# Kernel optimization log

Measured on AMD Instinct MI355X. Metric: run time of the kernel, lower is better.

## Reference

```python
import jax, jax.numpy as jnp
import numpy as np

DIM = 128
HEADS = 8
WS = 4  # window_size = size/11 = 44/11
HID = DIM * 4  # ffn_expansion_factor=4


def layernorm_cl(x, w, b):
    # WithBias LayerNorm over channel dim; x: (b,c,h,w)
    x3 = x.transpose(0, 2, 3, 1)  # b,h,w,c
    mu = x3.mean(-1, keepdims=True)
    var = ((x3 - mu) ** 2).mean(-1, keepdims=True)
    y = (x3 - mu) / jnp.sqrt(var + 1e-5) * w + b
    return y.transpose(0, 3, 1, 2)


def win_part(t, ws):
    # (b,c,h,w) -> (b*nh*nw, ws*ws, c), matching torch view/permute/contiguous
    b, c, h, w = t.shape
    t = t.reshape(b, c, h // ws, ws, w // ws, ws)
    t = t.transpose(0, 2, 4, 3, 5, 1)
    return t.reshape(b * (h // ws) * (w // ws), ws * ws, c)


def conv1x1(x, w):
    # w: (Cout, Cin, 1, 1)
    return jnp.einsum('bchw,oc->bohw', x, w[:, :, 0, 0])


def dwconv3(x, w):
    # depthwise 3x3, padding 1; w: (C,1,3,3)
    return jax.lax.conv_general_dilated(
        x, w, window_strides=(1, 1), padding=[(1, 1), (1, 1)],
        dimension_numbers=('NCHW', 'OIHW', 'NCHW'),
        feature_group_count=x.shape[1])


def setup_inputs() -> dict:
    key = jax.random.key(0)
    ks = jax.random.split(key, 10)
    b, c, h, w = 4, DIM, 176, 176
    inp = {
        'x': jax.random.normal(ks[0], (b, c, h, w), jnp.float32),
        'mask': jax.random.uniform(ks[1], (b, 1, 44, 44), jnp.float32),
        'edge': jax.random.normal(ks[2], (b, c, 44, 44), jnp.float32),
        'ln1_w': jnp.ones((c,), jnp.float32),
        'ln1_b': jnp.zeros((c,), jnp.float32),
        'Wq': jax.random.normal(ks[3], (c, c), jnp.float32) * 0.02,
        'Wk': jax.random.normal(ks[4], (c, c), jnp.float32) * 0.02,
        'Wv': jax.random.normal(ks[5], (c, c), jnp.float32) * 0.02,
        'ln2_w': jnp.ones((c,), jnp.float32),
        'ln2_b': jnp.zeros((c,), jnp.float32),
        'w_in': jax.random.normal(ks[6], (2 * HID, c, 1, 1), jnp.float32) * 0.02,
        'w_dw': jax.random.normal(ks[7], (2 * HID, 1, 3, 3), jnp.float32) * 0.1,
        'w_out': jax.random.normal(ks[8], (c, HID, 1, 1), jnp.float32) * 0.02,
    }
    return inp


def _forward(x, mask, edge, ln1_w, ln1_b, Wq, Wk, Wv, ln2_w, ln2_b, w_in, w_dw, w_out):
    b, c, h, w = x.shape
    d = c // HEADS
    scale = d ** (-0.5)

    # --- attention branch ---
    xn = layernorm_cl(x, ln1_w, ln1_b)
    x0 = xn

    edge_r = jax.image.resize(edge, (b, c, h, w), method='bilinear')
    mask_r = jax.image.resize(mask, (b, mask.shape[1], h, w), method='bilinear')

    q = win_part(edge_r, WS) @ Wq.T                 # (Bw, N, c)
    x0w = win_part(x0 * mask_r, WS)
    k = x0w @ Wk.T
    v = x0w @ Wv.T

    Bw, N = q.shape[0], q.shape[1]
    q = q.reshape(Bw, N, HEADS, d)
    k = k.reshape(Bw, N, HEADS, d)
    v = v.reshape(Bw, N, HEADS, d)

    # NB: faithful to original einsum -- contracts over heads axis, giving
    # per-token d x d channel attention.
    dots = jnp.einsum('bnij,bnik->bnjk', q, k) * scale  # (Bw, N, d, d)
    attn = jax.nn.softmax(dots, axis=-1)
    out = jnp.einsum('bnjk,bnik->bnij', attn, v)        # (Bw, N, HEADS, d)
    out = out.reshape(Bw, N, c)

    # faithful (non-inverse) window merge: view -> permute -> view
    out = out.reshape(b, h // WS, w // WS, WS * WS * c)
    out = out.transpose(0, 3, 1, 2).reshape(b, c, h, w)

    x = x + out

    # --- GDFN feedforward ---
    y = layernorm_cl(x, ln2_w, ln2_b)
    y = conv1x1(y, w_in)
    y = dwconv3(y, w_dw)
    y1, y2 = jnp.split(y, 2, axis=1)
    y = jax.nn.gelu(y1, approximate=False) * y2
    y = conv1x1(y, w_out)
    return x + y


def reference(x, mask, edge, ln1_w, ln1_b, Wq, Wk, Wv, ln2_w, ln2_b, w_in, w_dw, w_out):
    return _forward(x, mask, edge, ln1_w, ln1_b, Wq, Wk, Wv, ln2_w, ln2_b, w_in, w_dw, w_out)
```

## Files before the change

kernel.cpp:

```cpp
#include <hip/hip_runtime.h>
#include <hip/hip_bf16.h>
#include <math.h>

typedef __hip_bfloat16 bf16;
typedef short bf16x8 __attribute__((ext_vector_type(8)));
typedef short bf16x4 __attribute__((ext_vector_type(4)));
typedef float floatx4 __attribute__((ext_vector_type(4)));

#define YX 30976
#define NPOS (4*YX)

__device__ __forceinline__ float ldin(const void* p, size_t i, int bf) {
  return bf ? __bfloat162float(((const bf16*)p)[i]) : ((const float*)p)[i];
}

__device__ __forceinline__ void unpack8(bf16x8 v, float* f) {
  const unsigned* u = (const unsigned*)&v;
#pragma unroll
  for (int i = 0; i < 4; ++i) {
    f[2 * i]     = __uint_as_float(u[i] << 16);
    f[2 * i + 1] = __uint_as_float(u[i] & 0xffff0000u);
  }
}

__device__ __forceinline__ void glds16(const void* g, void* l) {
  __builtin_amdgcn_global_load_lds(
      (const __attribute__((address_space(1))) unsigned int*)g,
      (__attribute__((address_space(3))) unsigned int*)l, 16, 0, 0);
}

__device__ __forceinline__ void tap44(int o, int& i0, int& i1, float& f) {
  int t = o >> 2, r = o & 3;
  int base = (r < 2) ? (t - 1) : t;
  f = (r == 0) ? 0.625f : (r == 1) ? 0.875f : (r == 2) ? 0.125f : 0.375f;
  i0 = base < 0 ? 0 : base;
  i1 = (base + 1 > 43) ? 43 : base + 1;
}

__global__ void k_sniff(const unsigned* __restrict__ ln1w, int* __restrict__ flag) {
  if (threadIdx.x == 0 && blockIdx.x == 0)
    *flag = (*ln1w == 0x3F800000u) ? 0 : 1;
}

__global__ void __launch_bounds__(256) k_castw(
    const void* __restrict__ src, bf16* __restrict__ dst, int n,
    const int* __restrict__ flag) {
  int i = blockIdx.x * 256 + threadIdx.x;
  if (i >= n) return;
  int bf = *flag;
  dst[i] = bf ? ((const bf16*)src)[i]
              : __float2bfloat16(((const float*)src)[i]);
}

__global__ void __launch_bounds__(256) k_castdw(
    const void* __restrict__ src, bf16* __restrict__ dst,
    const int* __restrict__ flag) {
  int i = blockIdx.x * 256 + threadIdx.x;
  if (i >= 9216) return;
  int bf = *flag;
  int ch = i & 511, tap = (i >> 9) % 9, g = i / (512 * 9);
  float v = ldin(src, (size_t)(g * 512 + ch) * 9 + tap, bf);
  dst[(g * 9 + tap) * 512 + ch] = __float2bfloat16(v);
}

__global__ void __launch_bounds__(256) k_prep(
    const void* __restrict__ xin, const void* __restrict__ mask,
    const void* __restrict__ edge, const void* __restrict__ ln1w,
    const void* __restrict__ ln1b, const int* __restrict__ flag,
    bf16* __restrict__ e_buf, bf16* __restrict__ xm_buf,
    bf16* __restrict__ x_pm) {
  __shared__ float sP[4][64], ssP[4][64];
  __shared__ float smu[64], srstd[64], smv[64];
  __shared__ float slw[128], slb[128];
  __shared__ __align__(16) bf16 tileE[128 * 68];
  int bf = *flag;
  int tid = threadIdx.x;
  int p0 = blockIdx.x * 64;
  int b = p0 / YX, yx0 = p0 % YX;
  if (tid < 128) { slw[tid] = ldin(ln1w, tid, bf); slb[tid] = ldin(ln1b, tid, bf); }
  int pp = tid & 63, cq = tid >> 6;

  float vals[32], s = 0.f, ss = 0.f;
  {
    size_t base = ((size_t)(b * 128 + cq * 32)) * YX + yx0 + pp;
#pragma unroll
    for (int j = 0; j < 32; ++j) {
      float v = ldin(xin, base + (size_t)j * YX, bf);
      vals[j] = v; s += v; ss += v * v;
    }
  }
  sP[cq][pp] = s; ssP[cq][pp] = ss;
  __syncthreads();

  if (tid < 64) {
    float st  = sP[0][tid] + sP[1][tid] + sP[2][tid] + sP[3][tid];
    float sst = ssP[0][tid] + ssP[1][tid] + ssP[2][tid] + ssP[3][tid];
    float mu = st * (1.f / 128.f);
    float var = sst * (1.f / 128.f) - mu * mu;
    smu[tid] = mu;
    srstd[tid] = rsqrtf(fmaxf(var, 0.f) + 1e-5f);
    int gyx = yx0 + tid, y = gyx / 176, x = gyx % 176;
    int y0, y1, x0, x1; float fy, fx;
    tap44(y, y0, y1, fy); tap44(x, x0, x1, fx);
    size_t mb = (size_t)b * 1936;
    float m00 = ldin(mask, mb + y0 * 44 + x0, bf);
    float m01 = ldin(mask, mb + y0 * 44 + x1, bf);
    float m10 = ldin(mask, mb + y1 * 44 + x0, bf);
    float m11 = ldin(mask, mb + y1 * 44 + x1, bf);
    smv[tid] = (m00 * (1.f - fx) + m01 * fx) * (1.f - fy) +
               (m10 * (1.f - fx) + m11 * fx) * fy;
  }
  __syncthreads();

  {
    float mu = smu[pp], rstd = srstd[pp], mv = smv[pp];
    size_t ob = (size_t)(p0 + pp) * 128 + cq * 32;
#pragma unroll
    for (int j8 = 0; j8 < 4; ++j8) {
      bf16x8 xr, xmr;
#pragma unroll
      for (int i = 0; i < 8; ++i) {
        int j = j8 * 8 + i;
        float v = vals[j];
        int c = cq * 32 + j;
        ((bf16*)&xr)[i]  = __float2bfloat16(v);
        ((bf16*)&xmr)[i] = __float2bfloat16(((v - mu) * rstd * slw[c] + slb[c]) * mv);
      }
      *(bf16x8*)(x_pm + ob + j8 * 8)   = xr;
      *(bf16x8*)(xm_buf + ob + j8 * 8) = xmr;
    }
  }

  {
    int c = tid & 127, half = tid >> 7;
    size_t ebase = (size_t)(b * 128 + c) * 1936;
    int px = half * 32, pxend = px + 32;
    while (px < pxend) {
      int gyx = yx0 + px;
      int y = gyx / 176, x = gyx % 176;
      int seg = pxend - px;
      int rem = 176 - x;
      if (rem < seg) seg = rem;
      int y0, y1; float fy; tap44(y, y0, y1, fy);
      float fy0 = 1.f - fy;
      size_t r0 = ebase + (size_t)y0 * 44, r1 = ebase + (size_t)y1 * 44;
      int t = x >> 2;
      int tm = (t - 1 < 0) ? 0 : t - 1;
      int tp = (t + 1 > 43) ? 43 : t + 1;
      float Rm = fy0 * ldin(edge, r0 + tm, bf) + fy * ldin(edge, r1 + tm, bf);
      float R0 = fy0 * ldin(edge, r0 + t,  bf) + fy * ldin(edge, r1 + t,  bf);
      float Rp = fy0 * ldin(edge, r0 + tp, bf) + fy * ldin(edge, r1 + tp, bf);
      for (int g = 0; g < seg; g += 4) {
        bf16x4 pk;
        ((bf16*)&pk)[0] = __float2bfloat16(0.375f * Rm + 0.625f * R0);
        ((bf16*)&pk)[1] = __float2bfloat16(0.125f * Rm + 0.875f * R0);
        ((bf16*)&pk)[2] = __float2bfloat16(0.875f * R0 + 0.125f * Rp);
        ((bf16*)&pk)[3] = __float2bfloat16(0.625f * R0 + 0.375f * Rp);
        *(bf16x4*)&tileE[c * 68 + px + g] = pk;
        ++t;
        Rm = R0; R0 = Rp;
        int tn = (t + 1 > 43) ? 43 : t + 1;
        Rp = fy0 * ldin(edge, r0 + tn, bf) + fy * ldin(edge, r1 + tn, bf);
      }
      px += seg;
    }
  }
  __syncthreads();

  {
    size_t ob = (size_t)(p0 + pp) * 128 + cq * 32;
#pragma unroll
    for (int j8 = 0; j8 < 4; ++j8) {
      bf16x8 ev;
#pragma unroll
      for (int i = 0; i < 8; ++i)
        ((bf16*)&ev)[i] = tileE[(cq * 32 + j8 * 8 + i) * 68 + pp];
      *(bf16x8*)(e_buf + ob + j8 * 8) = ev;
    }
  }
}

__global__ void __launch_bounds__(384, 3) k_qkvattn(
    const bf16* __restrict__ E, const bf16* __restrict__ XM,
    const bf16* __restrict__ Wq, const bf16* __restrict__ Wk,
    const bf16* __restrict__ Wv, bf16* __restrict__ O) {
  __shared__ __align__(16) bf16 smem[32768];
  int tid = threadIdx.x;
  int wave = tid / 64, lane = tid & 63;
  int mat = wave >> 1, h = wave & 1;
  int l15 = lane & 15, quad = lane >> 4;
  int m0b = blockIdx.x * 64;

  const bf16* gA = (mat == 0) ? E : XM;
  const bf16* gW = (mat == 0) ? Wq : (mat == 1) ? Wk : Wv;

  floatx4 acc[4][4] = {};

#define STAGE(bb, kt)                                                          \
  {                                                                            \
    _Pragma("unroll")                                                          \
    for (int c = 0; c < 4; ++c)                                                \
      glds16(gW + (size_t)(h * 64 + c * 16 + l15) * 128 + (kt) + quad * 8,     \
             smem + (bb) + 4096 + mat * 4096 + (h * 4 + c) * 512);             \
    if (mat == 0) {                                                            \
      _Pragma("unroll")                                                        \
      for (int g = 0; g < 2; ++g) {                                            \
        int mm = h * 2 + g;                                                    \
        glds16(gA + (size_t)(m0b + mm * 16 + l15) * 128 + (kt) + quad * 8,     \
               smem + (bb) + mm * 512);                                        \
      }                                                                        \
    } else {                                                                   \
      int mm = wave - 2;                                                       \
      glds16(gA + (size_t)(m0b + mm * 16 + l15) * 128 + (kt) + quad * 8,       \
             smem + (bb) + 2048 + mm * 512);                                   \
    }                                                                          \
  }

  STAGE(0, 0);
  __syncthreads();

  int cur = 0;
  for (int t = 0; t < 4; ++t) {
    int nb = cur ^ 16384;
    if (t < 3) STAGE(nb, (t + 1) * 32);
    const bf16* sA = smem + cur + (mat ? 2048 : 0);
    const bf16* sW = smem + cur + 4096 + mat * 4096;
    bf16x8 af[4], bfr[4];
#pragma unroll
    for (int m = 0; m < 4; ++m)
      af[m] = *(const bf16x8*)(sA + m * 512 + lane * 8);
#pragma unroll
    for (int n = 0; n < 4; ++n)
      bfr[n] = *(const bf16x8*)(sW + (h * 4 + n) * 512 + lane * 8);
#pragma unroll
    for (int m = 0; m < 4; ++m)
#pragma unroll
      for (int n = 0; n < 4; ++n)
        acc[m][n] = __builtin_amdgcn_mfma_f32_16x16x32_bf16(bfr[n], af[m], acc[m][n], 0, 0, 0);
    __syncthreads();
    cur = nb;
  }
#undef STAGE

  if (mat < 2) {
    bf16* sT = smem + mat * 8192;
    int key = l15 & 7;
#pragma unroll
    for (int m = 0; m < 4; ++m) {
      int tokl = m * 16 + l15;
#pragma unroll
      for (int r = 0; r < 4; ++r) {
        int cidx = quad * 4 + r;
        bf16x4 o;
#pragma unroll
        for (int n = 0; n < 4; ++n) ((bf16*)&o)[n] = __float2bfloat16(acc[m][n][r]);
        *(bf16x4*)(sT + tokl * 128 + ((cidx ^ key) * 8) + h * 4) = o;
      }
    }
  } else {
    float* sVf = (float*)(smem + 16384);
    int key = l15 & 7;
#pragma unroll
    for (int m = 0; m < 4; ++m) {
      int tokl = m * 16 + l15;
#pragma unroll
      for (int n = 0; n < 4; ++n) {
        int ch4 = h * 16 + n * 4 + quad;
        floatx4 o;
#pragma unroll
        for (int r = 0; r < 4; ++r) o[r] = acc[m][n][r];
        *(floatx4*)(sVf + tokl * 128 + ((ch4 ^ key) << 2)) = o;
      }
    }
  }
  __syncthreads();

  const bf16* sQt = smem;
  const bf16* sKt = smem + 8192;
  const float* sVf = (const float*)(smem + 16384);
  for (int round = 0; round < 3; ++round) {
    int item = round * 384 + tid;
    if (item < 1024) {
      int tt = item >> 4, j = item & 15;
      int key = tt & 7;
      float qv[8];
      {
        bf16x8 q8 = *(const bf16x8*)(sQt + tt * 128 + ((j ^ key) * 8));
        unpack8(q8, qv);
      }
      float s[16], mx = -1e30f;
#pragma unroll
      for (int kk = 0; kk < 16; ++kk) {
        bf16x8 k8 = *(const bf16x8*)(sKt + tt * 128 + ((kk ^ key) * 8));
        float kv[8]; unpack8(k8, kv);
        float a = 0.f;
#pragma unroll
        for (int i = 0; i < 8; ++i) a += qv[i] * kv[i];
        a *= 0.25f;
        s[kk] = a; mx = fmaxf(mx, a);
      }
      float sum = 0.f;
#pragma unroll
      for (int kk = 0; kk < 16; ++kk) { s[kk] = __expf(s[kk] - mx); sum += s[kk]; }
      float inv = 1.f / sum;
      bf16x8 ov;
#pragma unroll
      for (int i = 0; i < 8; ++i) {
        float o = 0.f;
#pragma unroll
        for (int c4 = 0; c4 < 4; ++c4) {
          int ch4 = i * 4 + c4;
          floatx4 v4 = *(const floatx4*)(sVf + tt * 128 + ((ch4 ^ key) << 2));
#pragma unroll
          for (int r = 0; r < 4; ++r) o += s[c4 * 4 + r] * v4[r];
        }
        ((bf16*)&ov)[i] = __float2bfloat16(o * inv);
      }
      *(bf16x8*)(O + (size_t)(m0b + tt) * 128 + j * 8) = ov;
    }
  }
}

__global__ void __launch_bounds__(256) k_gemm2(
    const bf16* __restrict__ A, const bf16* __restrict__ W1,
    const bf16* __restrict__ W2, bf16* __restrict__ C1,
    bf16* __restrict__ C2) {
  __shared__ __align__(16) bf16 smem[20480];
  int tid = threadIdx.x;
  int wave = tid >> 6, lane = tid & 63;
  int row = lane & 15, kq8 = (lane >> 4) * 8;
  int m0b = blockIdx.x * 64;

  int srow = lane >> 2, scol = (lane & 3) * 8;
  const bf16* gA = A + (size_t)(m0b + wave * 16 + srow) * 128 + scol;
  const bf16* Wsrc = (wave < 2) ? W1 : W2;
  const bf16* gB = Wsrc + (size_t)((wave & 1) * 64 + srow) * 128 + scol;
  bf16* lA = smem + wave * 512;
  bf16* lB = smem + 2048 + wave * 2048;

  floatx4 acc[4][4] = {};
  glds16(gA, lA);
#pragma unroll
  for (int c = 0; c < 4; ++c) glds16(gB + c * 16 * 128, lB + c * 512);
  __syncthreads();

  int cur = 0;
  for (int t = 0; t < 4; ++t) {
    int nxt = cur ^ 1;
    if (t < 3) {
      const bf16* ga = gA + (t + 1) * 32;
      const bf16* gb = gB + (t + 1) * 32;
      glds16(ga, lA + nxt * 10240);
#pragma unroll
      for (int c = 0; c < 4; ++c)
        glds16(gb + c * 16 * 128, lB + nxt * 10240 + c * 512);
    }
    const bf16* sA = smem + cur * 10240;
    const bf16* sB = sA + 2048;
    bf16x8 af[4], bfr[4];
#pragma unroll
    for (int m = 0; m < 4; ++m)
      af[m] = *(const bf16x8*)(sA + (m * 16 + row) * 32 + kq8);
#pragma unroll
    for (int n = 0; n < 4; ++n)
      bfr[n] = *(const bf16x8*)(sB + (wave * 64 + n * 16 + row) * 32 + kq8);
#pragma unroll
    for (int m = 0; m < 4; ++m)
#pragma unroll
      for (int n = 0; n < 4; ++n)
        acc[m][n] = __builtin_amdgcn_mfma_f32_16x16x32_bf16(bfr[n], af[m], acc[m][n], 0, 0, 0);
    __syncthreads();
    cur = nxt;
  }

  bf16* dst = (wave < 2) ? C1 : C2;
  int j = lane & 15, quad = lane >> 4;
#pragma unroll
  for (int m = 0; m < 4; ++m) {
    size_t pb = (size_t)(m0b + m * 16 + j) * 128 + (wave & 1) * 64 + quad * 4;
#pragma unroll
    for (int n = 0; n < 4; ++n) {
      bf16x4 o;
#pragma unroll
      for (int r = 0; r < 4; ++r) ((bf16*)&o)[r] = __float2bfloat16(acc[m][n][r]);
      *(bf16x4*)(dst + pb + n * 16) = o;
    }
  }
}

__global__ void __launch_bounds__(256) k_merge(
    const bf16* __restrict__ AO2, const bf16* __restrict__ x_pm,
    const void* __restrict__ ln2w, const void* __restrict__ ln2b,
    const int* __restrict__ flag, bf16* __restrict__ resid,
    bf16* __restrict__ yln) {
  __shared__ __align__(16) bf16 stile[64 * 128];
  __shared__ float sP[4][64], ssP[4][64];
  __shared__ float smu[64], srstd[64];
  __shared__ float slw[128], slb[128];
  int bf = *flag;
  int tid = threadIdx.x;
  int bi = blockIdx.x;
  int iw0 = bi % 11, ih = (bi / 11) % 44, b = bi / 484;
  if (tid < 128) { slw[tid] = ldin(ln2w, tid, bf); slb[tid] = ldin(ln2b, tid, bf); }

#pragma unroll
  for (int q = 0; q < 4; ++q) {
    int idx = q * 256 + tid;
    int m = idx & 15, sp = idx >> 4;
    int dy = sp >> 4, wj = (sp >> 2) & 3, dx = sp & 3;
    int ys = ih * 4 + dy, xs = iw0 * 16 + wj * 4 + dx;
    bf16x8 v = *(const bf16x8*)(AO2 + (size_t)((b * 176 + ys) * 176 + xs) * 128 + m * 8);
    int opx = m * 4 + wj, n = dy * 4 + dx;
    *(bf16x8*)&stile[opx * 128 + (n ^ (opx & 15)) * 8] = v;
  }
  __syncthreads();

  int opx = tid & 63, cq = tid >> 6;
  int t = opx >> 2, wj = opx & 3;
  size_t p = (size_t)b * YX + t * 1936 + ih * 44 + iw0 * 4 + wj;
  float vals[32], s = 0.f, ss = 0.f;
#pragma unroll
  for (int j = 0; j < 4; ++j) {
    int nchunk = cq * 4 + j;
    bf16x8 av = *(const bf16x8*)&stile[opx * 128 + (nchunk ^ (opx & 15)) * 8];
    bf16x8 xv = *(const bf16x8*)(x_pm + p * 128 + cq * 32 + j * 8);
    float af[8], xf[8];
    unpack8(av, af); unpack8(xv, xf);
#pragma unroll
    for (int i = 0; i < 8; ++i) {
      float v = af[i] + xf[i];
      vals[j * 8 + i] = v; s += v; ss += v * v;
    }
  }
  sP[cq][opx] = s; ssP[cq][opx] = ss;
  __syncthreads();
  if (tid < 64) {
    float st  = sP[0][tid] + sP[1][tid] + sP[2][tid] + sP[3][tid];
    float sst = ssP[0][tid] + ssP[1][tid] + ssP[2][tid] + ssP[3][tid];
    float mu = st * (1.f / 128.f);
    float var = sst * (1.f / 128.f) - mu * mu;
    smu[tid] = mu;
    srstd[tid] = rsqrtf(fmaxf(var, 0.f) + 1e-5f);
  }
  __syncthreads();

  {
    float mu = smu[opx], rstd = srstd[opx];
    size_t ob = p * 128 + cq * 32;
#pragma unroll
    for (int j8 = 0; j8 < 4; ++j8) {
      bf16x8 rv, yv;
#pragma unroll
      for (int i = 0; i < 8; ++i) {
        int j = j8 * 8 + i;
        float v = vals[j];
        int c = cq * 32 + j;
        ((bf16*)&rv)[i] = __float2bfloat16(v);
        ((bf16*)&yv)[i] = __float2bfloat16((v - mu) * rstd * slw[c] + slb[c]);
      }
      *(bf16x8*)(resid + ob + j8 * 8) = rv;
      *(bf16x8*)(yln + ob + j8 * 8)   = yv;
    }
  }
}

__global__ void __launch_bounds__(256) k_dwgelu(
    const bf16* __restrict__ H1, const bf16* __restrict__ H2,
    const bf16* __restrict__ Wt, int j0, bf16* __restrict__ G) {
  int tid = blockIdx.x * 256 + threadIdx.x;
  int pos = tid >> 4, c8 = (tid & 15) * 8;
  int b = pos / YX, yx = pos % YX, y = yx / 176, x = yx % 176;
  float d1[8] = {}, d2[8] = {};
#pragma unroll
  for (int dy = 0; dy < 3; ++dy) {
    int ny = y + dy - 1;
    if (ny < 0 || ny > 175) continue;
#pragma unroll
    for (int dx = 0; dx < 3; ++dx) {
      int nx = x + dx - 1;
      if (nx < 0 || nx > 175) continue;
      int tap = dy * 3 + dx;
      size_t off = (size_t)(b * YX + ny * 176 + nx) * 128 + c8;
      float h1[8], h2[8], w1[8], w2[8];
      unpack8(*(const bf16x8*)(H1 + off), h1);
      unpack8(*(const bf16x8*)(H2 + off), h2);
      unpack8(*(const bf16x8*)(Wt + tap * 512 + j0 + c8), w1);
      unpack8(*(const bf16x8*)(Wt + (9 + tap) * 512 + j0 + c8), w2);
#pragma unroll
      for (int i = 0; i < 8; ++i) {
        d1[i] += w1[i] * h1[i];
        d2[i] += w2[i] * h2[i];
      }
    }
  }
  bf16x8 outv;
#pragma unroll
  for (int i = 0; i < 8; ++i) {
    float gl = 0.5f * d1[i] * (1.f + erff(d1[i] * 0.70710678118f));
    ((bf16*)&outv)[i] = __float2bfloat16(gl * d2[i]);
  }
  *(bf16x8*)(G + (size_t)pos * 512 + j0 + c8) = outv;
}

__global__ void __launch_bounds__(256) k_gemm_final(
    const bf16* __restrict__ G, const bf16* __restrict__ W,
    const bf16* __restrict__ resid, void* __restrict__ out,
    const int* __restrict__ flag) {
  __shared__ __align__(16) bf16 smem[16384];
  int tid = threadIdx.x;
  int wave = tid >> 6, lane = tid & 63;
  int row = lane & 15, kq8 = (lane >> 4) * 8;
  int wr = wave >> 1, wc = wave & 1;
  int m0b = blockIdx.x * 128;

  int srow = lane >> 2, scol = (lane & 3) * 8;
  const bf16* gA = G + (size_t)(m0b + wave * 32 + srow) * 512 + scol;
  const bf16* gB = W + (size_t)(wave * 32 + srow) * 512 + scol;
  bf16* lA = smem + wave * 1024;
  bf16* lB = smem + 4096 + wave * 1024;

  floatx4 acc[4][4] = {};
  glds16(gA, lA);            glds16(gA + 16 * 512, lA + 512);
  glds16(gB, lB);            glds16(gB + 16 * 512, lB + 512);
  __syncthreads();

  int cur = 0;
  for (int t = 0; t < 16; ++t) {
    int nxt = cur ^ 1;
    if (t < 15) {
      const bf16* ga = gA + (t + 1) * 32;
      const bf16* gb = gB + (t + 1) * 32;
      glds16(ga, lA + nxt * 8192);            glds16(ga + 16 * 512, lA + nxt * 8192 + 512);
      glds16(gb, lB + nxt * 8192);            glds16(gb + 16 * 512, lB + nxt * 8192 + 512);
    }
    const bf16* sA = smem + cur * 8192;
    const bf16* sB = sA + 4096;
    bf16x8 af[4], bfr[4];
#pragma unroll
    for (int m = 0; m < 4; ++m)
      af[m] = *(const bf16x8*)(sA + (wr * 64 + m * 16 + row) * 32 + kq8);
#pragma unroll
    for (int n = 0; n < 4; ++n)
      bfr[n] = *(const bf16x8*)(sB + (wc * 64 + n * 16 + row) * 32 + kq8);
#pragma unroll
    for (int m = 0; m < 4; ++m)
#pragma unroll
      for (int n = 0; n < 4; ++n)
        acc[m][n] = __builtin_amdgcn_mfma_f32_16x16x32_bf16(af[m], bfr[n], acc[m][n], 0, 0, 0);
    __syncthreads();
    cur = nxt;
  }

  {
    const bf16* gR = resid + (size_t)(m0b + wave * 32 + (lane >> 4)) * 128 + (lane & 15) * 8;
    bf16* lR = smem + wave * 32 * 128;
#pragma unroll
    for (int c = 0; c < 8; ++c)
      glds16(gR + (size_t)c * 4 * 128, lR + c * 4 * 128);
  }
  __syncthreads();

  int bfo = *flag;
  int b = m0b / YX, yx0 = m0b % YX;
  int j = lane & 15, quad = lane >> 4;
#pragma unroll
  for (int n = 0; n < 4; ++n) {
    int ch = wc * 64 + n * 16 + j;
    const bf16* rsl = smem + ch;
    size_t cb = (size_t)(b * 128 + ch) * YX + yx0;
#pragma unroll
    for (int m = 0; m < 4; ++m) {
      int pos = wr * 64 + m * 16 + quad * 4;
      float v[4];
#pragma unroll
      for (int r = 0; r < 4; ++r)
        v[r] = acc[m][n][r] + __bfloat162float(rsl[(pos + r) * 128]);
      if (bfo) {
        bf16x4 o;
#pragma unroll
        for (int r = 0; r < 4; ++r) ((bf16*)&o)[r] = __float2bfloat16(v[r]);
        *(bf16x4*)((bf16*)out + cb + pos) = o;
      } else {
        floatx4 o;
#pragma unroll
        for (int r = 0; r < 4; ++r) o[r] = v[r];
        *(floatx4*)((float*)out + cb + pos) = o;
      }
    }
  }
}

extern "C" void kernel_launch(void* const* d_in, const int* in_sizes, int n_in,
                              void* d_out, int out_size, void* d_ws, size_t ws_size,
                              hipStream_t stream) {
  const void* x    = d_in[0];
  const void* mask = d_in[1];
  const void* edge = d_in[2];
  const void* ln1w = d_in[3];
  const void* ln1b = d_in[4];
  const void* Wq   = d_in[5];
  const void* Wk   = d_in[6];
  const void* Wv   = d_in[7];
  const void* ln2w = d_in[8];
  const void* ln2b = d_in[9];
  const void* w_in = d_in[10];
  const void* w_dw = d_in[11];
  const void* w_out= d_in[12];

  char* ws = (char*)d_ws;
  const size_t SEG  = 31719424;
  const size_t GSZ  = 126877696;
  bf16* G     = (bf16*)(ws);
  bf16* B0    = (bf16*)(ws);
  bf16* B1    = (bf16*)(ws + GSZ);
  bf16* H1    = (bf16*)(ws + GSZ + SEG);
  bf16* H2    = (bf16*)(ws + GSZ + 2 * SEG);
  bf16* resid = (bf16*)(ws + GSZ + 3 * SEG);
  char* wsw   = ws + GSZ + 4 * SEG;
  bf16* wq_b   = (bf16*)(wsw);
  bf16* wk_b   = (bf16*)(wsw + 32768);
  bf16* wv_b   = (bf16*)(wsw + 65536);
  bf16* win_b  = (bf16*)(wsw + 98304);
  bf16* wout_b = (bf16*)(wsw + 98304 + 262144);
  bf16* wdwt_b = (bf16*)(wsw + 98304 + 262144 + 131072);
  int* flag    = (int*)(wsw + 98304 + 262144 + 131072 + 32768);

  k_sniff<<<1, 64, 0, stream>>>((const unsigned*)ln1w, flag);
  k_castw<<<64, 256, 0, stream>>>(Wq, wq_b, 16384, flag);
  k_castw<<<64, 256, 0, stream>>>(Wk, wk_b, 16384, flag);
  k_castw<<<64, 256, 0, stream>>>(Wv, wv_b, 16384, flag);
  k_castw<<<512, 256, 0, stream>>>(w_in, win_b, 131072, flag);
  k_castw<<<256, 256, 0, stream>>>(w_out, wout_b, 65536, flag);
  k_castdw<<<36, 256, 0, stream>>>(w_dw, wdwt_b, flag);

  k_prep<<<NPOS / 64, 256, 0, stream>>>(x, mask, edge, ln1w, ln1b, flag,
                                        B0, B1, H1 );
  k_qkvattn<<<NPOS / 64, 384, 0, stream>>>(B0, B1, wq_b, wk_b, wv_b, B0);
  k_merge<<<4 * 44 * 11, 256, 0, stream>>>(B0, H1 , ln2w, ln2b, flag,
                                           resid, B1);
  for (int j0 = 0; j0 < 512; j0 += 128) {
    k_gemm2<<<NPOS / 64, 256, 0, stream>>>(B1, win_b + (size_t)j0 * 128,
                                           win_b + (size_t)(512 + j0) * 128, H1, H2);
    k_dwgelu<<<NPOS * 16 / 256, 256, 0, stream>>>(H1, H2, wdwt_b, j0, G);
  }
  k_gemm_final<<<NPOS / 128, 256, 0, stream>>>(G, wout_b, resid, d_out, flag);
}
```

Measured before the change: 668.8 us.

## Split prep into separate edge-upsample and LayerNorm kernels with wider loads

The fused prep kernel is split into two kernels. k_edge handles one output row per block: it stages the two source edge rows in shared memory, transposed to channel-last, and writes vectorized bf16x8 interpolated outputs. k_ln1 now covers 128 pixels per block, and each thread loads two adjacent pixels with float2 or packed-bf16 loads, so global reads are wider and coalesced. This replaces the scalar strided edge gathers and the transposed tile store, at the cost of one extra kernel launch and higher register use in the LayerNorm kernel.

```diff
diff --git a/kernel.cpp b/kernel.cpp
--- a/kernel.cpp
+++ b/kernel.cpp
@@ -63,36 +63,46 @@
   dst[(g * 9 + tap) * 512 + ch] = __float2bfloat16(v);
 }
 
-__global__ void __launch_bounds__(256) k_prep(
+__global__ void __launch_bounds__(256) k_ln1(
     const void* __restrict__ xin, const void* __restrict__ mask,
-    const void* __restrict__ edge, const void* __restrict__ ln1w,
-    const void* __restrict__ ln1b, const int* __restrict__ flag,
-    bf16* __restrict__ e_buf, bf16* __restrict__ xm_buf,
-    bf16* __restrict__ x_pm) {
-  __shared__ float sP[4][64], ssP[4][64];
-  __shared__ float smu[64], srstd[64], smv[64];
+    const void* __restrict__ ln1w, const void* __restrict__ ln1b,
+    const int* __restrict__ flag,
+    bf16* __restrict__ xm_buf, bf16* __restrict__ x_pm) {
+  __shared__ float sP[4][128], ssP[4][128];
+  __shared__ float smu[128], srstd[128], smv[128];
   __shared__ float slw[128], slb[128];
-  __shared__ __align__(16) bf16 tileE[128 * 68];
   int bf = *flag;
   int tid = threadIdx.x;
-  int p0 = blockIdx.x * 64;
+  int p0 = blockIdx.x * 128;
   int b = p0 / YX, yx0 = p0 % YX;
   if (tid < 128) { slw[tid] = ldin(ln1w, tid, bf); slb[tid] = ldin(ln1b, tid, bf); }
   int pp = tid & 63, cq = tid >> 6;
 
-  float vals[32], s = 0.f, ss = 0.f;
+  float v0[32], v1[32];
+  float s0 = 0.f, ss0 = 0.f, s1 = 0.f, ss1 = 0.f;
   {
-    size_t base = ((size_t)(b * 128 + cq * 32)) * YX + yx0 + pp;
-#pragma unroll
-    for (int j = 0; j < 32; ++j) {
-      float v = ldin(xin, base + (size_t)j * YX, bf);
-      vals[j] = v; s += v; ss += v * v;
-    }
-  }
-  sP[cq][pp] = s; ssP[cq][pp] = ss;
-  __syncthreads();
-
-  if (tid < 64) {
+    size_t base = ((size_t)(b * 128 + cq * 32)) * YX + yx0 + pp * 2;
+    if (bf) {
+#pragma unroll
+      for (int j = 0; j < 32; ++j) {
+        unsigned u = *(const unsigned*)((const bf16*)xin + base + (size_t)j * YX);
+        float a = __uint_as_float(u << 16);
+        float c = __uint_as_float(u & 0xffff0000u);
+        v0[j] = a; v1[j] = c; s0 += a; ss0 += a * a; s1 += c; ss1 += c * c;
+      }
+    } else {
+#pragma unroll
+      for (int j = 0; j < 32; ++j) {
+        float2 f = *(const float2*)((const float*)xin + base + (size_t)j * YX);
+        v0[j] = f.x; v1[j] = f.y; s0 += f.x; ss0 += f.x * f.x; s1 += f.y; ss1 += f.y * f.y;
+      }
+    }
+  }
+  sP[cq][pp * 2] = s0;  sP[cq][pp * 2 + 1] = s1;
+  ssP[cq][pp * 2] = ss0; ssP[cq][pp * 2 + 1] = ss1;
+  __syncthreads();
+
+  if (tid < 128) {
     float st  = sP[0][tid] + sP[1][tid] + sP[2][tid] + sP[3][tid];
     float sst = ssP[0][tid] + ssP[1][tid] + ssP[2][tid] + ssP[3][tid];
     float mu = st * (1.f / 128.f);
@@ -112,71 +122,88 @@
   }
   __syncthreads();
 
-  {
-    float mu = smu[pp], rstd = srstd[pp], mv = smv[pp];
-    size_t ob = (size_t)(p0 + pp) * 128 + cq * 32;
-#pragma unroll
-    for (int j8 = 0; j8 < 4; ++j8) {
-      bf16x8 xr, xmr;
-#pragma unroll
-      for (int i = 0; i < 8; ++i) {
-        int j = j8 * 8 + i;
-        float v = vals[j];
-        int c = cq * 32 + j;
-        ((bf16*)&xr)[i]  = __float2bfloat16(v);
-        ((bf16*)&xmr)[i] = __float2bfloat16(((v - mu) * rstd * slw[c] + slb[c]) * mv);
-      }
-      *(bf16x8*)(x_pm + ob + j8 * 8)   = xr;
-      *(bf16x8*)(xm_buf + ob + j8 * 8) = xmr;
-    }
-  }
-
-  {
-    int c = tid & 127, half = tid >> 7;
-    size_t ebase = (size_t)(b * 128 + c) * 1936;
-    int px = half * 32, pxend = px + 32;
-    while (px < pxend) {
-      int gyx = yx0 + px;
-      int y = gyx / 176, x = gyx % 176;
-      int seg = pxend - px;
-      int rem = 176 - x;
-      if (rem < seg) seg = rem;
-      int y0, y1; float fy; tap44(y, y0, y1, fy);
-      float fy0 = 1.f - fy;
-      size_t r0 = ebase + (size_t)y0 * 44, r1 = ebase + (size_t)y1 * 44;
-      int t = x >> 2;
-      int tm = (t - 1 < 0) ? 0 : t - 1;
-      int tp = (t + 1 > 43) ? 43 : t + 1;
-      float Rm = fy0 * ldin(edge, r0 + tm, bf) + fy * ldin(edge, r1 + tm, bf);
-      float R0 = fy0 * ldin(edge, r0 + t,  bf) + fy * ldin(edge, r1 + t,  bf);
-      float Rp = fy0 * ldin(edge, r0 + tp, bf) + fy * ldin(edge, r1 + tp, bf);
-      for (int g = 0; g < seg; g += 4) {
-        bf16x4 pk;
-        ((bf16*)&pk)[0] = __float2bfloat16(0.375f * Rm + 0.625f * R0);
-        ((bf16*)&pk)[1] = __float2bfloat16(0.125f * Rm + 0.875f * R0);
-        ((bf16*)&pk)[2] = __float2bfloat16(0.875f * R0 + 0.125f * Rp);
-        ((bf16*)&pk)[3] = __float2bfloat16(0.625f * R0 + 0.375f * Rp);
-        *(bf16x4*)&tileE[c * 68 + px + g] = pk;
-        ++t;
-        Rm = R0; R0 = Rp;
-        int tn = (t + 1 > 43) ? 43 : t + 1;
-        Rp = fy0 * ldin(edge, r0 + tn, bf) + fy * ldin(edge, r1 + tn, bf);
-      }
-      px += seg;
-    }
-  }
-  __syncthreads();
-
-  {
-    size_t ob = (size_t)(p0 + pp) * 128 + cq * 32;
-#pragma unroll
-    for (int j8 = 0; j8 < 4; ++j8) {
-      bf16x8 ev;
-#pragma unroll
-      for (int i = 0; i < 8; ++i)
-        ((bf16*)&ev)[i] = tileE[(cq * 32 + j8 * 8 + i) * 68 + pp];
-      *(bf16x8*)(e_buf + ob + j8 * 8) = ev;
-    }
+#define WRITE_PX(K, VV)                                                        \
+  {                                                                            \
+    int px = pp * 2 + K;                                                       \
+    float mu = smu[px], rstd = srstd[px], mv = smv[px];                        \
+    size_t ob = (size_t)(p0 + px) * 128 + cq * 32;                             \
+    _Pragma("unroll")                                                          \
+    for (int j8 = 0; j8 < 4; ++j8) {                                           \
+      bf16x8 xr, xmr;                                                          \
+      _Pragma("unroll")                                                        \
+      for (int i = 0; i < 8; ++i) {                                            \
+        int j = j8 * 8 + i;                                                    \
+        float v = VV[j];                                                       \
+        int c = cq * 32 + j;                                                   \
+        ((bf16*)&xr)[i]  = __float2bfloat16(v);                                \
+        ((bf16*)&xmr)[i] = __float2bfloat16(((v - mu) * rstd * slw[c] + slb[c]) * mv); \
+      }                                                                        \
+      *(bf16x8*)(x_pm + ob + j8 * 8)   = xr;                                   \
+      *(bf16x8*)(xm_buf + ob + j8 * 8) = xmr;                                  \
+    }                                                                          \
+  }
+  WRITE_PX(0, v0)
+  WRITE_PX(1, v1)
+#undef WRITE_PX
+}
+
+__global__ void __launch_bounds__(256) k_edge(
+    const void* __restrict__ edge, const int* __restrict__ flag,
+    bf16* __restrict__ e_buf) {
+  __shared__ __align__(16) float sE[2 * 44 * 128];
+  int bf = *flag;
+  int tid = threadIdx.x;
+  int b = blockIdx.x / 176, y = blockIdx.x % 176;
+  int y0, y1; float fy; tap44(y, y0, y1, fy);
+  float fy0 = 1.f - fy;
+
+#pragma unroll
+  for (int r = 0; r < 2; ++r) {
+    int yr = r ? y1 : y0;
+#pragma unroll
+    for (int it = 0; it < 6; ++it) {
+      int idx = it * 256 + tid;
+      if (idx < 1408) {
+        int c = idx / 11, f4 = (idx % 11) * 4;
+        size_t src = (size_t)(b * 128 + c) * 1936 + yr * 44 + f4;
+        float4 v;
+        if (bf) {
+          bf16x4 bv = *(const bf16x4*)((const bf16*)edge + src);
+          v.x = __bfloat162float(((bf16*)&bv)[0]);
+          v.y = __bfloat162float(((bf16*)&bv)[1]);
+          v.z = __bfloat162float(((bf16*)&bv)[2]);
+          v.w = __bfloat162float(((bf16*)&bv)[3]);
+        } else {
+          v = *(const float4*)((const float*)edge + src);
+        }
+        float* d = sE + r * 5632 + f4 * 128 + c;
+        d[0] = v.x; d[128] = v.y; d[256] = v.z; d[384] = v.w;
+      }
+    }
+  }
+  __syncthreads();
+
+  const floatx4* sE4 = (const floatx4*)sE;
+  size_t rowbase = ((size_t)b * YX + (size_t)y * 176) * 128;
+#pragma unroll
+  for (int it = 0; it < 11; ++it) {
+    int chunk = it * 256 + tid;
+    int x = chunk >> 4, c8 = (chunk & 15) * 8;
+    int x0, x1; float fx; tap44(x, x0, x1, fx);
+    float fx0 = 1.f - fx;
+    float w00 = fy0 * fx0, w01 = fy0 * fx, w10 = fy * fx0, w11 = fy * fx;
+    int c4 = c8 >> 2;
+    floatx4 a0 = sE4[(0 * 44 + x0) * 32 + c4], a1 = sE4[(0 * 44 + x0) * 32 + c4 + 1];
+    floatx4 b0 = sE4[(0 * 44 + x1) * 32 + c4], b1 = sE4[(0 * 44 + x1) * 32 + c4 + 1];
+    floatx4 c0 = sE4[(44 + x0) * 32 + c4],     c1 = sE4[(44 + x0) * 32 + c4 + 1];
+    floatx4 d0 = sE4[(44 + x1) * 32 + c4],     d1 = sE4[(44 + x1) * 32 + c4 + 1];
+    bf16x8 o;
+#pragma unroll
+    for (int i = 0; i < 4; ++i) {
+      ((bf16*)&o)[i]     = __float2bfloat16(w00 * a0[i] + w01 * b0[i] + w10 * c0[i] + w11 * d0[i]);
+      ((bf16*)&o)[i + 4] = __float2bfloat16(w00 * a1[i] + w01 * b1[i] + w10 * c1[i] + w11 * d1[i]);
+    }
+    *(bf16x8*)(e_buf + rowbase + (size_t)x * 128 + c8) = o;
   }
 }
 
@@ -633,8 +660,9 @@
   k_castw<<<256, 256, 0, stream>>>(w_out, wout_b, 65536, flag);
   k_castdw<<<36, 256, 0, stream>>>(w_dw, wdwt_b, flag);
 
-  k_prep<<<NPOS / 64, 256, 0, stream>>>(x, mask, edge, ln1w, ln1b, flag,
-                                        B0, B1, H1 );
+  k_edge<<<4 * 176, 256, 0, stream>>>(edge, flag, B0);
+  k_ln1<<<NPOS / 128, 256, 0, stream>>>(x, mask, ln1w, ln1b, flag,
+                                        B1, H1 );
   k_qkvattn<<<NPOS / 64, 384, 0, stream>>>(B0, B1, wq_b, wk_b, wv_b, B0);
   k_merge<<<4 * 44 * 11, 256, 0, stream>>>(B0, H1 , ln2w, ln2b, flag,
                                            resid, B1);
```

Result: faster. 627.3 us (-6.2%).
